# Optimization experiments

Measured on AMD Instinct MI355X. Metric: run time of the kernel, lower is better.

## Reference

```python
import jax, jax.numpy as jnp
import numpy as np
from jax import lax

B, T1, T2, D, H = 4, 1024, 1024, 1024, 16
DK = D // H          # 64 per-head dim
K = 13               # conv kernel size
FF = 4 * D


def _ln(x, g, b, eps):
    mu = jnp.mean(x, axis=-1, keepdims=True)
    var = jnp.mean((x - mu) ** 2, axis=-1, keepdims=True)
    y = (x - mu) * lax.rsqrt(var + eps)
    if g is not None:
        y = y * g + b
    return y


def _conv1d(x, w, b):
    # x: (B, T, C) ; w: (O, C//H, K) grouped conv, 'same' padding
    y = lax.conv_general_dilated(
        x.transpose(0, 2, 1), w, window_strides=(1,),
        padding=[(K // 2, K // 2)],
        dimension_numbers=('NCH', 'OIH', 'NCH'),
        feature_group_count=H)
    return (y + b[None, :, None]).transpose(0, 2, 1)


def setup_inputs() -> dict:
    key = jax.random.key(0)
    ks = jax.random.split(key, 24)
    s = 0.02
    inp = {
        'noisy_feats': jax.random.normal(ks[0], (B, T1, D), jnp.float32),
        'clean_feats': jax.random.normal(ks[1], (B, T2, D), jnp.float32),
        't': jax.random.normal(ks[2], (B, D), jnp.float32),
        'ln_noisy_g': jnp.ones((D,), jnp.float32),
        'ln_noisy_b': jnp.zeros((D,), jnp.float32),
        'ln_clean_g': jnp.ones((D,), jnp.float32),
        'ln_clean_b': jnp.zeros((D,), jnp.float32),
        'ada_w': jax.random.normal(ks[3], (6 * D, D), jnp.float32) * s,
        'ada_b': jnp.zeros((6 * D,), jnp.float32),
        'wq': jax.random.normal(ks[4], (D, D // H, K), jnp.float32) * s,
        'bq': jnp.zeros((D,), jnp.float32),
        'wk': jax.random.normal(ks[5], (D, D // H, K), jnp.float32) * s,
        'bk': jnp.zeros((D,), jnp.float32),
        'wv': jax.random.normal(ks[6], (D, D // H, K), jnp.float32) * s,
        'bv': jnp.zeros((D,), jnp.float32),
        'fc_w': jax.random.normal(ks[7], (D, D), jnp.float32) * s,
        'fc_b': jnp.zeros((D,), jnp.float32),
        'ff_w1': jax.random.normal(ks[8], (FF, D), jnp.float32) * s,
        'ff_b1': jnp.zeros((FF,), jnp.float32),
        'ff_w2': jax.random.normal(ks[9], (D, FF), jnp.float32) * s,
        'ff_b2': jnp.zeros((D,), jnp.float32),
        'noisy_lengths': jax.random.randint(ks[10], (B,), 1, T1 + 1),
        'clean_lengths': jax.random.randint(ks[11], (B,), 1, T2 + 1),
    }
    return inp


def reference(noisy_feats, clean_feats, t,
              ln_noisy_g, ln_noisy_b, ln_clean_g, ln_clean_b,
              ada_w, ada_b, wq, bq, wk, bk, wv, bv, fc_w, fc_b,
              ff_w1, ff_b1, ff_w2, ff_b2,
              noisy_lengths, clean_lengths):
    # pre-norms (affine, eps=1e-5 torch default)
    noisy = _ln(noisy_feats, ln_noisy_g, ln_noisy_b, 1e-5)
    clean = _ln(clean_feats, ln_clean_g, ln_clean_b, 1e-5)

    # AdaLayerNormZero
    emb = jax.nn.silu(t) @ ada_w.T + ada_b                      # (B, 6D)
    shift_msa, scale_msa, gate_msa, shift_mlp, scale_mlp, gate_mlp = jnp.split(emb, 6, axis=1)
    normx = _ln(noisy, None, None, 1e-6) * (1.0 + scale_msa[:, None]) + shift_msa[:, None]

    # padding mask: True at pad positions (only context mask enters the scores)
    clean_mask = jnp.arange(T2)[None, :] >= clean_lengths[:, None]   # (B, T2)

    # grouped-conv QKV
    q = _conv1d(normx, wq, bq).reshape(B, T1, H, DK)
    k = _conv1d(clean, wk, bk).reshape(B, T2, H, DK)
    v = _conv1d(clean, wv, bv).reshape(B, T2, H, DK)

    scores = jnp.einsum('bqhd,bkhd->bhqk', q, k) / jnp.sqrt(jnp.float32(DK))
    scores = jnp.where(clean_mask[:, None, None, :], jnp.float32(-1e30), scores)
    p = jax.nn.softmax(scores, axis=-1)
    # rows where every key is masked -> zero (torch all_inf handling)
    all_masked = jnp.all(clean_mask, axis=-1)[:, None, None, None]
    p = jnp.where(all_masked, 0.0, p)

    out = jnp.einsum('bhqk,bkhd->bqhd', p, v).reshape(B, T1, D)
    out = out @ fc_w.T + fc_b

    x = noisy + gate_msa[:, None, :] * out
    n2 = _ln(x, None, None, 1e-6) * (1.0 + scale_mlp[:, None]) + shift_mlp[:, None]
    ff = jax.nn.gelu(n2 @ ff_w1.T + ff_b1, approximate=True) @ ff_w2.T + ff_b2
    return x + gate_mlp[:, None, :] * ff
```

## Files before the change

### kernel.cpp

```cpp
#include <hip/hip_runtime.h>
#include <hip/hip_bf16.h>

typedef __hip_bfloat16 bf16;
typedef __attribute__((ext_vector_type(8))) short short8;
typedef __attribute__((ext_vector_type(4))) float f32x4;

#define D_ 1024
#define SIXD 6144

__device__ __forceinline__ float bflo(unsigned int u){ union {unsigned int u; float f;} c; c.u = u << 16; return c.f; }
__device__ __forceinline__ float bfhi(unsigned int u){ union {unsigned int u; float f;} c; c.u = u & 0xFFFF0000u; return c.f; }
__device__ __forceinline__ float bload(const bf16* p){
  union {unsigned int u; float f;} c;
  c.u = ((unsigned int)(*reinterpret_cast<const unsigned short*>(p))) << 16;
  return c.f;
}
__device__ __forceinline__ bf16 bstore(float f){ return __float2bfloat16(f); }
__device__ __forceinline__ unsigned short bf16bits(float f){
  bf16 b = __float2bfloat16(f);
  return *reinterpret_cast<unsigned short*>(&b);
}

__device__ __forceinline__ void gload16(const bf16* g, bf16* l){
  __builtin_amdgcn_global_load_lds((const __attribute__((address_space(1))) unsigned int*)g,
                                   (__attribute__((address_space(3))) unsigned int*)l, 16, 0, 0);
}

template<int ISBF>
__device__ __forceinline__ float ild(const void* p, size_t i){
  if (ISBF) return bload((const bf16*)p + i);
  return ((const float*)p)[i];
}

__device__ __forceinline__ float block_sum(float v, float* sh4){
  #pragma unroll
  for (int o = 32; o; o >>= 1) v += __shfl_down(v, o);
  __syncthreads();
  int lane = threadIdx.x & 63, wid = threadIdx.x >> 6;
  if (lane == 0) sh4[wid] = v;
  __syncthreads();
  return sh4[0] + sh4[1] + sh4[2] + sh4[3];
}

__global__ void detect_kernel(const unsigned int* g, int* flag){
  unsigned int u = *g;
  *flag = (u == 0x3F803F80u) ? 1 : 0;
}

template<int ISBF>
__device__ __forceinline__ void emb_body(const void* T, const void* AW, const void* AB,
                                         float* E, float* st){
  int b = blockIdx.y;
  int tid = threadIdx.x;
  for (int c = tid; c < D_; c += 256) {
    float x = ild<ISBF>(T, (size_t)b*D_ + c);
    st[c] = x / (1.f + expf(-x));
  }
  __syncthreads();
  int wid = tid >> 6, lane = tid & 63;
  int j = blockIdx.x * 4 + wid;
  float dot = 0.f;
  for (int c = lane; c < D_; c += 64) dot += ild<ISBF>(AW, (size_t)j*D_ + c) * st[c];
  #pragma unroll
  for (int o = 32; o; o >>= 1) dot += __shfl_down(dot, o);
  if (lane == 0) E[b*SIXD + j] = dot + ild<ISBF>(AB, j);
}
__global__ __launch_bounds__(256) void emb_kernel(const void* T, const void* AW, const void* AB,
                                                  const int* flagp, float* E){
  __shared__ float st[D_];
  if (*flagp) emb_body<1>(T, AW, AB, E, st); else emb_body<0>(T, AW, AB, E, st);
}

template<int ISBF>
__device__ __forceinline__ void ln_noisy_body(const void* X, const void* G, const void* Bt,
                                              const float* E, bf16* xbuf, bf16* normx, float* sh4){
  int r = blockIdx.x; int b = r >> 10;
  int tid = threadIdx.x; int c0 = tid * 4;
  size_t base = (size_t)r*D_ + c0;
  float f0 = ild<ISBF>(X, base+0), f1 = ild<ISBF>(X, base+1);
  float f2 = ild<ISBF>(X, base+2), f3 = ild<ISBF>(X, base+3);
  float mean = block_sum(f0+f1+f2+f3, sh4) * (1.f/D_);
  float var  = block_sum(f0*f0+f1*f1+f2*f2+f3*f3, sh4) * (1.f/D_) - mean*mean;
  float rstd = rsqrtf(fmaxf(var, 0.f) + 1e-5f);
  float y0 = (f0-mean)*rstd*ild<ISBF>(G,c0+0) + ild<ISBF>(Bt,c0+0);
  float y1 = (f1-mean)*rstd*ild<ISBF>(G,c0+1) + ild<ISBF>(Bt,c0+1);
  float y2 = (f2-mean)*rstd*ild<ISBF>(G,c0+2) + ild<ISBF>(Bt,c0+2);
  float y3 = (f3-mean)*rstd*ild<ISBF>(G,c0+3) + ild<ISBF>(Bt,c0+3);
  bf16* xo = xbuf + base;
  xo[0]=bstore(y0); xo[1]=bstore(y1); xo[2]=bstore(y2); xo[3]=bstore(y3);
  float m2 = block_sum(y0+y1+y2+y3, sh4) * (1.f/D_);
  float v2 = block_sum(y0*y0+y1*y1+y2*y2+y3*y3, sh4) * (1.f/D_) - m2*m2;
  float rstd2 = rsqrtf(fmaxf(v2, 0.f) + 1e-6f);
  const float* eb = E + b*SIXD;
  bf16* o = normx + base;
  o[0] = bstore((y0-m2)*rstd2*(1.f+eb[1024+c0+0]) + eb[c0+0]);
  o[1] = bstore((y1-m2)*rstd2*(1.f+eb[1024+c0+1]) + eb[c0+1]);
  o[2] = bstore((y2-m2)*rstd2*(1.f+eb[1024+c0+2]) + eb[c0+2]);
  o[3] = bstore((y3-m2)*rstd2*(1.f+eb[1024+c0+3]) + eb[c0+3]);
}
__global__ __launch_bounds__(256) void ln_noisy_fused(const void* X, const void* G, const void* Bt,
                                                      const float* E, bf16* xbuf, bf16* normx,
                                                      const int* flagp){
  __shared__ float sh4[4];
  if (*flagp) ln_noisy_body<1>(X,G,Bt,E,xbuf,normx,sh4); else ln_noisy_body<0>(X,G,Bt,E,xbuf,normx,sh4);
}

template<int ISBF>
__device__ __forceinline__ void ln_clean_body(const void* X, const void* G, const void* Bt,
                                              bf16* Y, float* sh4){
  int r = blockIdx.x;
  int tid = threadIdx.x; int c0 = tid * 4;
  size_t base = (size_t)r*D_ + c0;
  float f0 = ild<ISBF>(X, base+0), f1 = ild<ISBF>(X, base+1);
  float f2 = ild<ISBF>(X, base+2), f3 = ild<ISBF>(X, base+3);
  float mean = block_sum(f0+f1+f2+f3, sh4) * (1.f/D_);
  float var  = block_sum(f0*f0+f1*f1+f2*f2+f3*f3, sh4) * (1.f/D_) - mean*mean;
  float rstd = rsqrtf(fmaxf(var, 0.f) + 1e-5f);
  bf16* o = Y + base;
  o[0] = bstore((f0-mean)*rstd*ild<ISBF>(G,c0+0) + ild<ISBF>(Bt,c0+0));
  o[1] = bstore((f1-mean)*rstd*ild<ISBF>(G,c0+1) + ild<ISBF>(Bt,c0+1));
  o[2] = bstore((f2-mean)*rstd*ild<ISBF>(G,c0+2) + ild<ISBF>(Bt,c0+2));
  o[3] = bstore((f3-mean)*rstd*ild<ISBF>(G,c0+3) + ild<ISBF>(Bt,c0+3));
}
__global__ __launch_bounds__(256) void ln_clean_kernel(const void* X, const void* G, const void* Bt,
                                                       bf16* Y, const int* flagp){
  __shared__ float sh4[4];
  if (*flagp) ln_clean_body<1>(X,G,Bt,Y,sh4); else ln_clean_body<0>(X,G,Bt,Y,sh4);
}

__global__ __launch_bounds__(256) void ln2_kernel(const bf16* __restrict__ X, const float* __restrict__ E,
                                                  bf16* __restrict__ Y){
  __shared__ float sh4[4];
  int r = blockIdx.x; int b = r >> 10;
  int tid = threadIdx.x; int c0 = tid * 4;
  uint2 u = *reinterpret_cast<const uint2*>(X + (size_t)r*D_ + c0);
  float f0 = bflo(u.x), f1 = bfhi(u.x), f2 = bflo(u.y), f3 = bfhi(u.y);
  float mean = block_sum(f0+f1+f2+f3, sh4) * (1.f/D_);
  float var  = block_sum(f0*f0+f1*f1+f2*f2+f3*f3, sh4) * (1.f/D_) - mean*mean;
  float rstd = rsqrtf(fmaxf(var, 0.f) + 1e-6f);
  const float* eb = E + b*SIXD;
  bf16* o = Y + (size_t)r*D_ + c0;
  o[0] = bstore((f0-mean)*rstd*(1.f+eb[4096+c0+0]) + eb[3072+c0+0]);
  o[1] = bstore((f1-mean)*rstd*(1.f+eb[4096+c0+1]) + eb[3072+c0+1]);
  o[2] = bstore((f2-mean)*rstd*(1.f+eb[4096+c0+2]) + eb[3072+c0+2]);
  o[3] = bstore((f3-mean)*rstd*(1.f+eb[4096+c0+3]) + eb[3072+c0+3]);
}

template<int ISBF>
__device__ __forceinline__ void wtrans_body(const void* W, bf16* Wtr){
  size_t idx = (size_t)blockIdx.x * 256 + threadIdx.x;
  int si = idx & 63;
  size_t r = idx >> 6;
  int o = (int)(r & 63); r >>= 6;
  int k = (int)(r % 13);
  int g = (int)(r / 13);
  int i = si ^ ((o & 7) << 3);
  Wtr[idx] = bstore(ild<ISBF>(W, ((size_t)(g*64 + o)*64 + i)*13 + k));
}
__global__ __launch_bounds__(256) void conv_wtrans(const void* W, bf16* Wtr, const int* flagp){
  if (*flagp) wtrans_body<1>(W, Wtr); else wtrans_body<0>(W, Wtr);
}

template<int ISBF>
__device__ __forceinline__ void wconv_body(const void* W, bf16* o, int n){
  for (int i = blockIdx.x*256 + threadIdx.x; i < n; i += gridDim.x*256)
    o[i] = bstore(ild<ISBF>(W, (size_t)i));
}
__global__ __launch_bounds__(256) void wconv_kernel(const void* W, bf16* o, int n, const int* flagp){
  if (*flagp) wconv_body<1>(W, o, n); else wconv_body<0>(W, o, n);
}

template<int ISBF>
__device__ __forceinline__ void convl_body(const bf16* __restrict__ X,
                                           const bf16* __restrict__ Wtr, const void* Bias,
                                           bf16* __restrict__ Y,
                                           bf16* ws, bf16* xs){
  int tid = threadIdx.x;
  int wave = tid >> 6, lane = tid & 63;
  int fr = lane & 15, fq = lane >> 4;
  int t0 = blockIdx.x * 256;
  int g = blockIdx.y, b = blockIdx.z;
  const bf16* Wg = Wtr + (size_t)g*53248;
  #pragma unroll
  for (int p = 0; p < 13; ++p)
    gload16(Wg + ((size_t)p*512 + tid)*8, ws + (p*512 + tid)*8);
  const bf16* xg = X + ((size_t)b*1024)*D_ + g*64;
  for (int idx = tid; idx < 268*8; idx += 512) {
    int row = idx >> 3, q = idx & 7;
    int t = t0 - 6 + row;
    uint4 v = make_uint4(0,0,0,0);
    if (t >= 0 && t < 1024)
      v = *reinterpret_cast<const uint4*>(xg + (size_t)t*D_ + q*8);
    *reinterpret_cast<uint4*>(&xs[row*72 + q*8]) = v;
  }
  __syncthreads();
  f32x4 acc[2][4];
  #pragma unroll
  for (int i = 0; i < 2; ++i)
    #pragma unroll
    for (int j = 0; j < 4; ++j) acc[i][j] = (f32x4){0.f,0.f,0.f,0.f};
  int wrow = wave * 32;
  const bf16* a0 = xs + (wrow + fr)*72 + fq*8;
  for (int k = 0; k < 13; ++k) {
    const bf16* wk_ = ws + (k*64 + fr)*64;
    const bf16* ar = a0 + k*72;
    #pragma unroll
    for (int h = 0; h < 2; ++h) {
      int swz = (h*32 + fq*8) ^ ((fr & 7) << 3);
      short8 af0 = *reinterpret_cast<const short8*>(ar + h*32);
      short8 af1 = *reinterpret_cast<const short8*>(ar + 16*72 + h*32);
      #pragma unroll
      for (int tn = 0; tn < 4; ++tn) {
        short8 bv = *reinterpret_cast<const short8*>(wk_ + tn*1024 + swz);
        acc[0][tn] = __builtin_amdgcn_mfma_f32_16x16x32_bf16(af0, bv, acc[0][tn], 0,0,0);
        acc[1][tn] = __builtin_amdgcn_mfma_f32_16x16x32_bf16(af1, bv, acc[1][tn], 0,0,0);
      }
    }
  }
  #pragma unroll
  for (int tm = 0; tm < 2; ++tm) {
    #pragma unroll
    for (int tn = 0; tn < 4; ++tn) {
      int oc = g*64 + tn*16 + fr;
      float bb = ild<ISBF>(Bias, oc);
      #pragma unroll
      for (int r = 0; r < 4; ++r) {
        int tt = t0 + wrow + tm*16 + fq*4 + r;
        Y[((size_t)(b*1024 + tt))*D_ + oc] = bstore(acc[tm][tn][r] + bb);
      }
    }
  }
}
__global__ __launch_bounds__(512) void conv_lds(const bf16* X, const bf16* Wtr, const void* Bias,
                                                bf16* Y, const int* flagp){
  extern __shared__ bf16 smem[];
  bf16* ws = smem;
  bf16* xs = smem + 53248;
  if (*flagp) convl_body<1>(X, Wtr, Bias, Y, ws, xs);
  else        convl_body<0>(X, Wtr, Bias, Y, ws, xs);
}
#define CONV_LDS_BYTES ((53248 + 268*72) * 2)

__global__ __launch_bounds__(256) void attn_mfma(const bf16* __restrict__ Q, const bf16* __restrict__ Kb,
                                                 const bf16* __restrict__ V, const int* __restrict__ lens,
                                                 bf16* __restrict__ O){
  __shared__ bf16 qs[64*72];
  __shared__ bf16 ks[64*72];
  __shared__ bf16 vt[64*72];
  __shared__ bf16 ps[4][16*72];
  int tid = threadIdx.x;
  int wave = tid >> 6, lane = tid & 63;
  int fr = lane & 15, fq = lane >> 4;
  int qb = blockIdx.x, h = blockIdx.y, b = blockIdx.z;
  int len = lens[b]; len = len < 0 ? 0 : (len > 1024 ? 1024 : len);
  {
    int row = tid >> 2, col = (tid & 3) * 16;
    const bf16* src = Q + ((size_t)(b*1024 + qb*64 + row))*D_ + h*64 + col;
    *reinterpret_cast<uint4*>(&qs[row*72 + col])     = *reinterpret_cast<const uint4*>(src);
    *reinterpret_cast<uint4*>(&qs[row*72 + col + 8]) = *reinterpret_cast<const uint4*>(src + 8);
  }
  __syncthreads();
  short8 bq0 = *reinterpret_cast<const short8*>(&qs[(wave*16 + fr)*72 + fq*8]);
  short8 bq1 = *reinterpret_cast<const short8*>(&qs[(wave*16 + fr)*72 + 32 + fq*8]);
  f32x4 oacc[4];
  #pragma unroll
  for (int t = 0; t < 4; ++t) oacc[t] = (f32x4){0.f,0.f,0.f,0.f};
  float m_ = -1e30f, l_ = 0.f;
  int krow = tid >> 2, kcol = (tid & 3) * 16;
  int vk = (tid >> 3) * 2, vcol = (tid & 7) * 8;
  const bf16* kg = Kb + ((size_t)b*1024)*D_ + h*64;
  const bf16* vg = V  + ((size_t)b*1024)*D_ + h*64;
  for (int k0 = 0; k0 < len; k0 += 64) {
    uint4 kv0 = make_uint4(0,0,0,0), kv1 = make_uint4(0,0,0,0);
    uint4 va = make_uint4(0,0,0,0), vb = make_uint4(0,0,0,0);
    if (k0 + krow < len) {
      kv0 = *reinterpret_cast<const uint4*>(kg + (size_t)(k0+krow)*D_ + kcol);
      kv1 = *reinterpret_cast<const uint4*>(kg + (size_t)(k0+krow)*D_ + kcol + 8);
    }
    if (k0 + vk < len)     va = *reinterpret_cast<const uint4*>(vg + (size_t)(k0+vk)*D_ + vcol);
    if (k0 + vk + 1 < len) vb = *reinterpret_cast<const uint4*>(vg + (size_t)(k0+vk+1)*D_ + vcol);
    __syncthreads();
    *reinterpret_cast<uint4*>(&ks[krow*72 + kcol])     = kv0;
    *reinterpret_cast<uint4*>(&ks[krow*72 + kcol + 8]) = kv1;
    {
      union { uint4 u; unsigned short s[8]; } ca, cb; ca.u = va; cb.u = vb;
      #pragma unroll
      for (int j = 0; j < 8; ++j) {
        unsigned int w = ((unsigned int)cb.s[j] << 16) | (unsigned int)ca.s[j];
        int d = vcol + j;
        int blk = ((vk >> 3) ^ ((d >> 3) & 7)) << 3;
        *reinterpret_cast<unsigned int*>(&vt[d*72 + blk + (vk & 7)]) = w;
      }
    }
    __syncthreads();
    f32x4 s[4];
    #pragma unroll
    for (int f = 0; f < 4; ++f) {
      short8 ak0 = *reinterpret_cast<const short8*>(&ks[(f*16 + fr)*72 + fq*8]);
      short8 ak1 = *reinterpret_cast<const short8*>(&ks[(f*16 + fr)*72 + 32 + fq*8]);
      s[f] = (f32x4){0.f,0.f,0.f,0.f};
      s[f] = __builtin_amdgcn_mfma_f32_16x16x32_bf16(ak0, bq0, s[f], 0,0,0);
      s[f] = __builtin_amdgcn_mfma_f32_16x16x32_bf16(ak1, bq1, s[f], 0,0,0);
    }
    float p[4][4];
    float pmax = -1e30f;
    #pragma unroll
    for (int f = 0; f < 4; ++f)
      #pragma unroll
      for (int r = 0; r < 4; ++r) {
        float sv = (k0 + f*16 + fq*4 + r < len) ? s[f][r]*0.125f : -1e30f;
        p[f][r] = sv;
        pmax = fmaxf(pmax, sv);
      }
    pmax = fmaxf(pmax, __shfl_xor(pmax, 16));
    pmax = fmaxf(pmax, __shfl_xor(pmax, 32));
    float mnew = fmaxf(m_, pmax);
    float alpha = __expf(m_ - mnew);
    float psum = 0.f;
    #pragma unroll
    for (int f = 0; f < 4; ++f)
      #pragma unroll
      for (int r = 0; r < 4; ++r) {
        float pv = __expf(p[f][r] - mnew);
        p[f][r] = pv;
        psum += pv;
      }
    psum += __shfl_xor(psum, 16);
    psum += __shfl_xor(psum, 32);
    l_ = l_*alpha + psum;
    m_ = mnew;
    #pragma unroll
    for (int f = 0; f < 4; ++f) {
      unsigned int lo = ((unsigned int)bf16bits(p[f][1]) << 16) | (unsigned int)bf16bits(p[f][0]);
      unsigned int hi = ((unsigned int)bf16bits(p[f][3]) << 16) | (unsigned int)bf16bits(p[f][2]);
      unsigned int* pp = reinterpret_cast<unsigned int*>(&ps[wave][fr*72 + f*16 + fq*4]);
      pp[0] = lo; pp[1] = hi;
    }
    float aq[4];
    #pragma unroll
    for (int r = 0; r < 4; ++r) aq[r] = __shfl(alpha, fq*4 + r);
    #pragma unroll
    for (int tn = 0; tn < 4; ++tn)
      #pragma unroll
      for (int r = 0; r < 4; ++r) oacc[tn][r] *= aq[r];
    short8 ap0 = *reinterpret_cast<const short8*>(&ps[wave][fr*72 + fq*8]);
    short8 ap1 = *reinterpret_cast<const short8*>(&ps[wave][fr*72 + 32 + fq*8]);
    #pragma unroll
    for (int tn = 0; tn < 4; ++tn) {
      int d = tn*16 + fr;
      int sw = (d >> 3) & 7;
      short8 bv0 = *reinterpret_cast<const short8*>(&vt[d*72 + ((fq     ^ sw) << 3)]);
      short8 bv1 = *reinterpret_cast<const short8*>(&vt[d*72 + (((4+fq) ^ sw) << 3)]);
      oacc[tn] = __builtin_amdgcn_mfma_f32_16x16x32_bf16(ap0, bv0, oacc[tn], 0,0,0);
      oacc[tn] = __builtin_amdgcn_mfma_f32_16x16x32_bf16(ap1, bv1, oacc[tn], 0,0,0);
    }
  }
  float linv = (l_ > 0.f) ? 1.f/l_ : 0.f;
  float iq[4];
  #pragma unroll
  for (int r = 0; r < 4; ++r) iq[r] = __shfl(linv, fq*4 + r);
  #pragma unroll
  for (int r = 0; r < 4; ++r) {
    int q = qb*64 + wave*16 + fq*4 + r;
    bf16* op = O + ((size_t)(b*1024 + q))*D_ + h*64 + fr;
    #pragma unroll
    for (int tn = 0; tn < 4; ++tn)
      op[tn*16] = bstore(oacc[tn][r] * iq[r]);
  }
}

template<int ISBF>
__device__ __forceinline__ void mgemm_body(const bf16* __restrict__ A, const bf16* __restrict__ W,
                                           const void* bias, int bofs,
                                           int K, int ldA, int ldW, int Nst, int mode, int gate_ofs,
                                           bf16* xbuf, const float* emb, void* outb,
                                           bf16* As, bf16* Bs){
  int tid = threadIdx.x;
  int nwg = gridDim.x * gridDim.y;
  int flat = blockIdx.y * gridDim.x + blockIdx.x;
  int swz = (flat & 7) * (nwg >> 3) + (flat >> 3);
  int bx = swz % gridDim.x, by = swz / gridDim.x;
  int m0 = by * 128, n0 = bx * 128;
  int wave = tid >> 6, lane = tid & 63;
  int wr = wave >> 2, wc = wave & 3;
  int fr = lane & 15, fq = lane >> 4;
  int srow = tid >> 2, skc = (tid & 3) * 8;
  const bf16* Ag = A + (size_t)(m0 + srow)*ldA + skc;
  const bf16* Wg = W + (size_t)(n0 + srow)*ldW + skc;
  bf16* Asl = As + tid*8;
  bf16* Bsl = Bs + tid*8;
  const bf16* Afr = As + (wr*64 + fr)*32 + fq*8;
  const bf16* Bfr = Bs + (wc*32 + fr)*32 + fq*8;
  f32x4 acc[4][2];
  #pragma unroll
  for (int i = 0; i < 4; ++i)
    #pragma unroll
    for (int j = 0; j < 2; ++j) acc[i][j] = (f32x4){0.f,0.f,0.f,0.f};
  int nt = K >> 6;
  gload16(Ag,       Asl);
  gload16(Ag + 32,  Asl + 4096);
  gload16(Wg,       Bsl);
  gload16(Wg + 32,  Bsl + 4096);
  gload16(Ag + 64,  Asl + 8192);
  gload16(Ag + 96,  Asl + 8192 + 4096);
  gload16(Wg + 64,  Bsl + 8192);
  gload16(Wg + 96,  Bsl + 8192 + 4096);
  for (int t = 0; t < nt; ++t) {
    if (t + 2 < nt) {
      int k2 = (t + 2) << 6;
      int bo = ((t + 2) & 3) * 8192;
      gload16(Ag + k2,      Asl + bo);
      gload16(Ag + k2 + 32, Asl + bo + 4096);
      gload16(Wg + k2,      Bsl + bo);
      gload16(Wg + k2 + 32, Bsl + bo + 4096);
      asm volatile("s_waitcnt vmcnt(8)" ::: "memory");
    } else if (t + 1 < nt) {
      asm volatile("s_waitcnt vmcnt(4)" ::: "memory");
    } else {
      asm volatile("s_waitcnt vmcnt(0)" ::: "memory");
    }
    __builtin_amdgcn_sched_barrier(0);
    __builtin_amdgcn_s_barrier();
    __builtin_amdgcn_sched_barrier(0);
    int co = (t & 3) * 8192;
    #pragma unroll
    for (int ks = 0; ks < 2; ++ks) {
      short8 af[4], bfv[2];
      #pragma unroll
      for (int tm = 0; tm < 4; ++tm) af[tm] = *reinterpret_cast<const short8*>(Afr + co + ks*4096 + tm*16*32);
      #pragma unroll
      for (int tn = 0; tn < 2; ++tn) bfv[tn] = *reinterpret_cast<const short8*>(Bfr + co + ks*4096 + tn*16*32);
      #pragma unroll
      for (int tm = 0; tm < 4; ++tm)
        #pragma unroll
        for (int tn = 0; tn < 2; ++tn)
          acc[tm][tn] = __builtin_amdgcn_mfma_f32_16x16x32_bf16(af[tm], bfv[tn], acc[tm][tn], 0, 0, 0);
    }
  }
  #pragma unroll
  for (int tm = 0; tm < 4; ++tm) {
    #pragma unroll
    for (int tn = 0; tn < 2; ++tn) {
      int nn = n0 + wc*32 + tn*16 + fr;
      float bv = bias ? ild<ISBF>(bias, (size_t)(bofs + nn)) : 0.f;
      #pragma unroll
      for (int r = 0; r < 4; ++r) {
        int mm = m0 + wr*64 + tm*16 + fq*4 + r;
        float v = acc[tm][tn][r] + bv;
        const float* eb = emb + (mm >> 10)*SIXD;
        if (mode == 1) {
          float tt = 0.7978845608028654f * (v + 0.044715f * v * v * v);
          ((bf16*)outb)[(size_t)mm*Nst + nn] = bstore(0.5f * v * (1.f + tanhf(tt)));
        } else if (mode == 2) {
          size_t xi = (size_t)mm*1024 + nn;
          xbuf[xi] = bstore(bload(xbuf + xi) + eb[gate_ofs + nn] * v);
        } else {
          size_t xi = (size_t)mm*1024 + nn;
          float rr = bload(xbuf + xi) + eb[gate_ofs + nn] * v;
          if (ISBF) ((bf16*)outb)[xi] = bstore(rr);
          else      ((float*)outb)[xi] = rr;
        }
      }
    }
  }
}
__global__ __launch_bounds__(512) void mgemm_kernel(const bf16* A, const bf16* W,
                                                    const void* bias, int bofs,
                                                    int K, int ldA, int ldW, int Nst, int mode, int gate_ofs,
                                                    bf16* xbuf, const float* emb, void* outb,
                                                    const int* flagp){
  extern __shared__ bf16 gsm[];
  bf16* As = gsm;
  bf16* Bs = gsm + 32768;
  if (*flagp) mgemm_body<1>(A,W,bias,bofs,K,ldA,ldW,Nst,mode,gate_ofs,xbuf,emb,outb,As,Bs);
  else        mgemm_body<0>(A,W,bias,bofs,K,ldA,ldW,Nst,mode,gate_ofs,xbuf,emb,outb,As,Bs);
}
#define MGEMM_LDS_BYTES (65536 * 2)

extern "C" void kernel_launch(void* const* d_in, const int* in_sizes, int n_in,
                              void* d_out, int out_size, void* d_ws, size_t ws_size,
                              hipStream_t stream) {
  (void)in_sizes; (void)n_in; (void)out_size; (void)ws_size;
  const void* noisy = d_in[0];
  const void* clean = d_in[1];
  const void* t     = d_in[2];
  const void* lng   = d_in[3];
  const void* lnb   = d_in[4];
  const void* lcg   = d_in[5];
  const void* lcb   = d_in[6];
  const void* ada_w = d_in[7];
  const void* ada_b = d_in[8];
  const void* wq    = d_in[9];
  const void* bq    = d_in[10];
  const void* wk    = d_in[11];
  const void* bk    = d_in[12];
  const void* wv    = d_in[13];
  const void* bv    = d_in[14];
  const void* fc_w  = d_in[15];
  const void* fc_b  = d_in[16];
  const void* ff_w1 = d_in[17];
  const void* ff_b1 = d_in[18];
  const void* ff_w2 = d_in[19];
  const void* ff_b2 = d_in[20];
  const int*  clen  = (const int*)d_in[22];

  char* w = (char*)d_ws;
  int*   flagp = (int*)w;
  float* embp  = (float*)(w + 4096);
  bf16*  xbuf  = (bf16*)(w + 102400);
  bf16*  normx = (bf16*)(w + 8491008);
  bf16*  cleanb= (bf16*)(w + 16879616);
  bf16*  qb    = (bf16*)(w + 25268224);
  bf16*  kbuf  = (bf16*)(w + 33656832);
  bf16*  vbuf  = (bf16*)(w + 42045440);
  bf16*  wqtr  = (bf16*)(w + 50434048);
  bf16*  wktr  = (bf16*)(w + 52137984);
  bf16*  wvtr  = (bf16*)(w + 53841920);
  bf16*  ff1h  = qb;
  bf16*  attno = cleanb;
  bf16*  n2b   = normx;
  bf16*  fc_wb = wqtr;
  bf16*  ffw1b = vbuf;
  bf16*  ffw2b = cleanb;

  detect_kernel<<<1, 1, 0, stream>>>((const unsigned int*)lng, flagp);
  emb_kernel<<<dim3(1536, 4), 256, 0, stream>>>(t, ada_w, ada_b, flagp, embp);
  ln_noisy_fused<<<4096, 256, 0, stream>>>(noisy, lng, lnb, embp, xbuf, normx, flagp);
  ln_clean_kernel<<<4096, 256, 0, stream>>>(clean, lcg, lcb, cleanb, flagp);
  conv_wtrans<<<3328, 256, 0, stream>>>(wq, wqtr, flagp);
  conv_wtrans<<<3328, 256, 0, stream>>>(wk, wktr, flagp);
  conv_wtrans<<<3328, 256, 0, stream>>>(wv, wvtr, flagp);
  conv_lds<<<dim3(4, 16, 4), 512, CONV_LDS_BYTES, stream>>>(normx,  wqtr, bq, qb,   flagp);
  conv_lds<<<dim3(4, 16, 4), 512, CONV_LDS_BYTES, stream>>>(cleanb, wktr, bk, kbuf, flagp);
  conv_lds<<<dim3(4, 16, 4), 512, CONV_LDS_BYTES, stream>>>(cleanb, wvtr, bv, vbuf, flagp);
  wconv_kernel<<<1024, 256, 0, stream>>>(fc_w, fc_wb, 1048576, flagp);
  attn_mfma<<<dim3(16, 16, 4), 256, 0, stream>>>(qb, kbuf, vbuf, clen, attno);
  wconv_kernel<<<2048, 256, 0, stream>>>(ff_w1, ffw1b, 4194304, flagp);
  mgemm_kernel<<<dim3(8, 32), 512, MGEMM_LDS_BYTES, stream>>>(attno, fc_wb, fc_b, 0,
                                                1024, 1024, 1024, 1024, 2, 2048, xbuf, embp, nullptr, flagp);
  wconv_kernel<<<2048, 256, 0, stream>>>(ff_w2, ffw2b, 4194304, flagp);
  ln2_kernel<<<4096, 256, 0, stream>>>(xbuf, embp, n2b);
  mgemm_kernel<<<dim3(16, 32), 512, MGEMM_LDS_BYTES, stream>>>(n2b, ffw1b, ff_b1, 0,
                                                 1024, 1024, 1024, 2048, 1, 0, xbuf, embp, ff1h, flagp);
  mgemm_kernel<<<dim3(8, 32), 512, MGEMM_LDS_BYTES, stream>>>(ff1h, ffw2b, ff_b2, 0,
                                                2048, 2048, 4096, 1024, 2, 5120, xbuf, embp, nullptr, flagp);
  mgemm_kernel<<<dim3(16, 32), 512, MGEMM_LDS_BYTES, stream>>>(n2b, ffw1b + (size_t)2048*1024, ff_b1, 2048,
                                                 1024, 1024, 1024, 2048, 1, 0, xbuf, embp, ff1h, flagp);
  mgemm_kernel<<<dim3(8, 32), 512, MGEMM_LDS_BYTES, stream>>>(ff1h, ffw2b + 2048, nullptr, 0,
                                                2048, 2048, 4096, 1024, 3, 5120, xbuf, embp, d_out, flagp);
}
```

Measured before the change: 461.7 us.

## Remap GEMM tiles per XCD quadrant and unroll K loop by four with setprio

Each XCD is now given a contiguous 2D quadrant of output tiles instead of a strided 1D swizzle, so blocks on the same XCD share A rows and W columns in that XCD's L2. The main K loop is unrolled by four so LDS buffer offsets become compile-time constants, and the tail is peeled into its own loop. The MFMA section is wrapped in s_setprio so math waves get scheduling priority. The new mapping assumes gridDim.x is divisible by 2 and gridDim.y by 4, and nt must be a multiple of 4 and at least 4.

```diff
diff --git a/kernel.cpp b/kernel.cpp
--- a/kernel.cpp
+++ b/kernel.cpp
@@ -376,10 +376,14 @@
                                            bf16* xbuf, const float* emb, void* outb,
                                            bf16* As, bf16* Bs){
   int tid = threadIdx.x;
-  int nwg = gridDim.x * gridDim.y;
   int flat = blockIdx.y * gridDim.x + blockIdx.x;
-  int swz = (flat & 7) * (nwg >> 3) + (flat >> 3);
-  int bx = swz % gridDim.x, by = swz / gridDim.x;
+  int cx = gridDim.x >> 1;
+  int cy = gridDim.y >> 2;
+  int xcd = flat & 7;
+  int idx = flat >> 3;
+  int rby = idx / cx, rbx = idx - rby*cx;
+  int by = (xcd & 3)*cy + rby;
+  int bx = (xcd >> 2)*cx + rbx;
   int m0 = by * 128, n0 = bx * 128;
   int wave = tid >> 6, lane = tid & 63;
   int wr = wave >> 2, wc = wave & 3;
@@ -405,36 +409,75 @@
   gload16(Ag + 96,  Asl + 8192 + 4096);
   gload16(Wg + 64,  Bsl + 8192);
   gload16(Wg + 96,  Bsl + 8192 + 4096);
-  for (int t = 0; t < nt; ++t) {
-    if (t + 2 < nt) {
-      int k2 = (t + 2) << 6;
-      int bo = ((t + 2) & 3) * 8192;
-      gload16(Ag + k2,      Asl + bo);
-      gload16(Ag + k2 + 32, Asl + bo + 4096);
-      gload16(Wg + k2,      Bsl + bo);
-      gload16(Wg + k2 + 32, Bsl + bo + 4096);
+  int tmain = nt - 4;
+  for (int t4 = 0; t4 < tmain; t4 += 4) {
+    const bf16* Agt = Ag + ((t4 + 2) << 6);
+    const bf16* Wgt = Wg + ((t4 + 2) << 6);
+    #pragma unroll
+    for (int u = 0; u < 4; ++u) {
+      const int bo = ((u + 2) & 3) * 8192;
+      gload16(Agt + (u << 6),      Asl + bo);
+      gload16(Agt + (u << 6) + 32, Asl + bo + 4096);
+      gload16(Wgt + (u << 6),      Bsl + bo);
+      gload16(Wgt + (u << 6) + 32, Bsl + bo + 4096);
       asm volatile("s_waitcnt vmcnt(8)" ::: "memory");
-    } else if (t + 1 < nt) {
-      asm volatile("s_waitcnt vmcnt(4)" ::: "memory");
-    } else {
-      asm volatile("s_waitcnt vmcnt(0)" ::: "memory");
-    }
-    __builtin_amdgcn_sched_barrier(0);
-    __builtin_amdgcn_s_barrier();
-    __builtin_amdgcn_sched_barrier(0);
-    int co = (t & 3) * 8192;
-    #pragma unroll
-    for (int ks = 0; ks < 2; ++ks) {
-      short8 af[4], bfv[2];
-      #pragma unroll
-      for (int tm = 0; tm < 4; ++tm) af[tm] = *reinterpret_cast<const short8*>(Afr + co + ks*4096 + tm*16*32);
-      #pragma unroll
-      for (int tn = 0; tn < 2; ++tn) bfv[tn] = *reinterpret_cast<const short8*>(Bfr + co + ks*4096 + tn*16*32);
-      #pragma unroll
-      for (int tm = 0; tm < 4; ++tm)
+      __builtin_amdgcn_sched_barrier(0);
+      __builtin_amdgcn_s_barrier();
+      __builtin_amdgcn_sched_barrier(0);
+      const int co = u * 8192;
+      __builtin_amdgcn_s_setprio(1);
+      #pragma unroll
+      for (int ks = 0; ks < 2; ++ks) {
+        short8 af[4], bfv[2];
         #pragma unroll
-        for (int tn = 0; tn < 2; ++tn)
-          acc[tm][tn] = __builtin_amdgcn_mfma_f32_16x16x32_bf16(af[tm], bfv[tn], acc[tm][tn], 0, 0, 0);
+        for (int tm = 0; tm < 4; ++tm) af[tm] = *reinterpret_cast<const short8*>(Afr + co + ks*4096 + tm*16*32);
+        #pragma unroll
+        for (int tn = 0; tn < 2; ++tn) bfv[tn] = *reinterpret_cast<const short8*>(Bfr + co + ks*4096 + tn*16*32);
+        #pragma unroll
+        for (int tm = 0; tm < 4; ++tm)
+          #pragma unroll
+          for (int tn = 0; tn < 2; ++tn)
+            acc[tm][tn] = __builtin_amdgcn_mfma_f32_16x16x32_bf16(af[tm], bfv[tn], acc[tm][tn], 0, 0, 0);
+      }
+      __builtin_amdgcn_s_setprio(0);
+    }
+  }
+  {
+    const bf16* Agt = Ag + ((tmain + 2) << 6);
+    const bf16* Wgt = Wg + ((tmain + 2) << 6);
+    #pragma unroll
+    for (int u = 0; u < 4; ++u) {
+      if (u < 2) {
+        const int bo = ((u + 2) & 3) * 8192;
+        gload16(Agt + (u << 6),      Asl + bo);
+        gload16(Agt + (u << 6) + 32, Asl + bo + 4096);
+        gload16(Wgt + (u << 6),      Bsl + bo);
+        gload16(Wgt + (u << 6) + 32, Bsl + bo + 4096);
+        asm volatile("s_waitcnt vmcnt(8)" ::: "memory");
+      } else if (u == 2) {
+        asm volatile("s_waitcnt vmcnt(4)" ::: "memory");
+      } else {
+        asm volatile("s_waitcnt vmcnt(0)" ::: "memory");
+      }
+      __builtin_amdgcn_sched_barrier(0);
+      __builtin_amdgcn_s_barrier();
+      __builtin_amdgcn_sched_barrier(0);
+      const int co = u * 8192;
+      __builtin_amdgcn_s_setprio(1);
+      #pragma unroll
+      for (int ks = 0; ks < 2; ++ks) {
+        short8 af[4], bfv[2];
+        #pragma unroll
+        for (int tm = 0; tm < 4; ++tm) af[tm] = *reinterpret_cast<const short8*>(Afr + co + ks*4096 + tm*16*32);
+        #pragma unroll
+        for (int tn = 0; tn < 2; ++tn) bfv[tn] = *reinterpret_cast<const short8*>(Bfr + co + ks*4096 + tn*16*32);
+        #pragma unroll
+        for (int tm = 0; tm < 4; ++tm)
+          #pragma unroll
+          for (int tn = 0; tn < 2; ++tn)
+            acc[tm][tn] = __builtin_amdgcn_mfma_f32_16x16x32_bf16(af[tm], bfv[tn], acc[tm][tn], 0, 0, 0);
+      }
+      __builtin_amdgcn_s_setprio(0);
     }
   }
   #pragma unroll
```

Result: faster. 445.2 us (-3.6%).
